# Performance work log

Measured on AMD Instinct MI355X. Metric: run time of the kernel, lower is better.

The kernel has to match this reference:

```python
import jax, jax.numpy as jnp
import numpy as np
import math

ALPHA = 0.5
DT = 0.1
DX = 1.0 / 128
KAPPA = 0.01

LAPL_OPS = [[[[0.34520446044393, 0.309591078922457, 0.34520446044393],
              [0.309591078922457, -2.619182157203629, 0.309591078922457],
              [0.34520446044393, 0.309591078922457, 0.34520446044393]]]]

T, C, H, W = 512, 2, 257, 257


def setup_inputs() -> dict:
    key = jax.random.key(0)
    k1, k2 = jax.random.split(key)
    output = jax.random.normal(k1, (T, C, H, W), dtype=jnp.float32)
    f1 = jax.random.normal(k2, (T, 1, H, W), dtype=jnp.float32)
    lap_kernel = jnp.asarray(LAPL_OPS, dtype=jnp.float32)  # (1,1,3,3), OIHW
    return {"output": output, "f1": f1, "lap_kernel": lap_kernel}


def _l1_weight_matrix(T_):
    # L1 fractional-derivative weights: w[j] = (j+1)^(1-a) - j^(1-a), j = 0..T-2
    a = ALPHA
    j = jnp.arange(T_ - 1, dtype=jnp.float32)
    w = (j + 1.0) ** (1.0 - a) - j ** (1.0 - a)  # w[0] = 1
    # dvec[m] = w[m-1] - w[m] for m >= 1 (m = i - k)
    dvec = jnp.concatenate([jnp.zeros((1,), jnp.float32), w[:-1] - w[1:]])
    i = jnp.arange(T_)[:, None]
    k = jnp.arange(T_)[None, :]
    diff = jnp.clip(i - k, 0, T_ - 2)
    M = jnp.where((i >= 1) & (k == i), 1.0, 0.0)                               # w0 * u_i
    M = M + jnp.where((k >= 1) & (k < i), -dvec[diff], 0.0)                    # -(w[i-k-1]-w[i-k]) u_k
    M = M + jnp.where((k == 0) & (i >= 1), -w[jnp.clip(i - 1, 0, T_ - 2)], 0.0)  # -w[i-1] u_0
    return M  # row 0 is all zeros, matching b[0] = 0


def reference(output, f1, lap_kernel):
    T_, _, H_, W_ = output.shape
    u = output[:, 0:1, :, :]                      # (T,1,H,W)
    u_flat = u.reshape(T_, H_ * W_)               # (T, N)

    # fractional time derivative as a single triangular matmul over time
    M = _l1_weight_matrix(T_)
    scale = DT ** (-ALPHA) / math.gamma(2.0 - ALPHA)
    D = (scale * (M @ u_flat)).reshape(T_, 1, H_, W_)

    # 3x3 Laplacian, VALID conv, divided by dx^2
    lap_u = jax.lax.conv_general_dilated(
        u, lap_kernel, window_strides=(1, 1), padding='VALID',
        dimension_numbers=('NCHW', 'OIHW', 'NCHW')) / (DX ** 2)

    res = (D[:, :, 1:-1, 1:-1] - KAPPA * lap_u
           + u[:, :, 1:-1, 1:-1] - f1[:, :, 1:-1, 1:-1])
    return jnp.mean(res ** 2)
```

## Files before the change

### kernel.cpp

```cpp
#include <hip/hip_runtime.h>

#define TT    512
#define WW    257
#define HWSZ  (WW*WW)
#define IMG2  (2*HWSZ)
#define SCALE 3.5682482323055424f
#define KD    163.84f

typedef short bf16x8 __attribute__((ext_vector_type(8)));
typedef short bf16x4 __attribute__((ext_vector_type(4)));
typedef float f32x4  __attribute__((ext_vector_type(4)));
typedef unsigned int u32x4 __attribute__((ext_vector_type(4)));

__device__ __forceinline__ float wf(int j) {
    return sqrtf((float)(j + 1)) - sqrtf((float)j);
}
__device__ __forceinline__ float mcoef(int i, int k) {
    if (i == 0 || k > i) return 0.f;
    if (k == i) return 1.f;
    if (k == 0) return -wf(i - 1);
    int d = i - k;
    return wf(d) - wf(d - 1);
}
__device__ __forceinline__ unsigned short f2b(float f) {
    unsigned u = __float_as_uint(f);
    return (unsigned short)((u + 0x7FFFu + ((u >> 16) & 1u)) >> 16);
}
__device__ __forceinline__ float b2f(unsigned short h) {
    return __uint_as_float(((unsigned)h) << 16);
}

__global__ __launch_bounds__(256)
void build_m(unsigned short* __restrict__ M, float* __restrict__ d_out) {
    int i = blockIdx.x;
    if (i == 0 && threadIdx.x == 0) *d_out = 0.f;
    for (int k = threadIdx.x; k < TT; k += 256)
        M[i * TT + k] = f2b(mcoef(i, k));
}

__global__ __launch_bounds__(512, 2)
void fused(const float* __restrict__ uin, const float* __restrict__ f1p,
           const float* __restrict__ lapk, const unsigned short* __restrict__ Mb,
           float* __restrict__ d_out)
{
    __shared__ unsigned short uS[2][128][64];
    __shared__ unsigned short sS[2][64][136];
    __shared__ float red[8];

    const int tid  = threadIdx.x;
    const int w    = tid >> 6;
    const int lane = tid & 63;
    const int lr   = lane & 15;
    const int lg   = lane >> 4;

    const int bid = blockIdx.x;
    const int wg  = (bid & 7) * 64 + (bid >> 3);
    const int xt  = wg >> 7;
    const int ypb = wg & 127;
    const int Y0  = 1 + 2 * ypb;
    const int c0  = xt * 64;
    const bool validB = (Y0 + 1) <= 255;

    const float ka = lapk[0], kb = lapk[1], kc = lapk[4];

    f32x4 acc0[8][2], acc1[8][2];
    #pragma unroll
    for (int a = 0; a < 8; ++a) {
        acc0[a][0] = (f32x4)0.f; acc0[a][1] = (f32x4)0.f;
        acc1[a][0] = (f32x4)0.f; acc1[a][1] = (f32x4)0.f;
    }

    const bool pad = (c0 + lane) == 255;
    const int  i00 = 32 * w;
    const int  i01 = 480 - 32 * w;
    const int  ec0 = w >> 1;
    const int  ec1 = (15 - w) >> 1;
    float lsum = 0.f;

    float a0[8], a1[8], a2[8], a3[8], fA[8], fB[8], ee;
    const int tl = lane >> 3, code = lane & 7, side = code >> 2, rj = code & 3;
    const size_t geoff = (size_t)tl * IMG2 + (size_t)(Y0 - 1 + rj) * WW
                       + (side ? c0 + 65 : c0);

    auto LOADR = [&](int c) {
        const int tb = 64 * c + 8 * w;
        const float* pu = uin + (size_t)tb * IMG2 + (size_t)(Y0 - 1) * WW + (c0 + 1) + lane;
        const float* pf = f1p + (size_t)tb * HWSZ + (size_t)Y0 * WW + (c0 + 1) + lane;
        #pragma unroll
        for (int rr = 0; rr < 8; ++rr) {
            const float* qu = pu + (size_t)rr * IMG2;
            a0[rr] = qu[0]; a1[rr] = qu[WW]; a2[rr] = qu[2 * WW]; a3[rr] = qu[3 * WW];
            fA[rr] = pf[(size_t)rr * HWSZ];
            fB[rr] = pf[(size_t)rr * HWSZ + WW];
        }
        ee = uin[(size_t)tb * IMG2 + geoff];
    };

    auto STAGE = [&](int b) {
        float e1  = __shfl(ee, lane + 1, 64);
        float e2  = __shfl(ee, lane + 2, 64);
        float QeX = fmaf(ka, ee + e2, kb * e1);
        u32x4 upA, upB;
        #pragma unroll
        for (int rr = 0; rr < 8; ++rr) {
            float PA = a0[rr] + a2[rr];
            float QA = fmaf(ka, PA, kb * a1[rr]);
            float RA = fmaf(kb, PA, kc * a1[rr]);
            float PB = a1[rr] + a3[rr];
            float QB = fmaf(ka, PB, kb * a2[rr]);
            float RB = fmaf(kb, PB, kc * a2[rr]);
            float qmA = __shfl(QA, lane - 1, 64), qpA = __shfl(QA, lane + 1, 64);
            float qmB = __shfl(QB, lane - 1, 64), qpB = __shfl(QB, lane + 1, 64);
            float eA0 = __shfl(QeX, 8 * rr,     64), eA1 = __shfl(QeX, 8 * rr + 4, 64);
            float eB0 = __shfl(QeX, 8 * rr + 1, 64), eB1 = __shfl(QeX, 8 * rr + 5, 64);
            if (lane == 0)  { qmA = eA0; qmB = eB0; }
            if (lane == 63) { qpA = eA1; qpB = eB1; }
            float lapA = qmA + qpA + RA;
            float lapB = qmB + qpB + RB;
            float sA = a1[rr] - fmaf(KD, lapA, fA[rr]);
            float sB_ = a2[rr] - fmaf(KD, lapB, fB[rr]);
            unsigned short uAv = pad ? (unsigned short)0 : f2b(a1[rr]);
            unsigned short sAv = pad ? (unsigned short)0 : f2b(sA);
            unsigned short uBv = (pad || !validB) ? (unsigned short)0 : f2b(a2[rr]);
            unsigned short sBv = (pad || !validB) ? (unsigned short)0 : f2b(sB_);
            sS[b][8 * w + rr][lane]      = sAv;
            sS[b][8 * w + rr][64 + lane] = sBv;
            if (rr & 1) { upA[rr >> 1] |= ((unsigned)uAv) << 16; upB[rr >> 1] |= ((unsigned)uBv) << 16; }
            else        { upA[rr >> 1]  = (unsigned)uAv;         upB[rr >> 1]  = (unsigned)uBv; }
        }
        *(u32x4*)&uS[b][lane]     [(w ^ (lane & 7)) * 8] = upA;
        *(u32x4*)&uS[b][64 + lane][(w ^ (lane & 7)) * 8] = upB;
    };

    auto EPI = [&](f32x4 (&acc)[8][2], int b, int lbase) {
        #pragma unroll
        for (int mi = 0; mi < 8; ++mi)
            #pragma unroll
            for (int nj = 0; nj < 2; ++nj) {
                bf16x4 sv = *(const bf16x4*)&sS[b][lbase + 16 * nj + lr][16 * mi + 4 * lg];
                #pragma unroll
                for (int r = 0; r < 4; ++r) {
                    float res = SCALE * acc[mi][nj][r] + b2f((unsigned short)sv[r]);
                    lsum += res * res;
                }
            }
    };

    LOADR(0);
    for (int c = 0; c < 8; ++c) {
        const int b = c & 1;

        bf16x8 m0a[2], m0b[2], m1a[2], m1b[2];
        #pragma unroll
        for (int sub = 0; sub < 2; ++sub) {
            const int s_ = 2 * c + sub;
            if (s_ <= w) {
                const unsigned short* mp0 = Mb + (size_t)(i00 + lr) * TT + 32 * s_ + 8 * lg;
                m0a[sub] = *(const bf16x8*)mp0; m0b[sub] = *(const bf16x8*)(mp0 + 16 * TT);
            }
            if (s_ <= 15 - w) {
                const unsigned short* mp1 = Mb + (size_t)(i01 + lr) * TT + 32 * s_ + 8 * lg;
                m1a[sub] = *(const bf16x8*)mp1; m1b[sub] = *(const bf16x8*)(mp1 + 16 * TT);
            }
        }
        __builtin_amdgcn_sched_barrier(0);

        STAGE(b);
        if (c < 7) LOADR(c + 1);

        __builtin_amdgcn_sched_barrier(0);
        asm volatile("s_waitcnt lgkmcnt(0)");
        __builtin_amdgcn_sched_barrier(0);
        __builtin_amdgcn_s_barrier();
        __builtin_amdgcn_sched_barrier(0);

        __builtin_amdgcn_s_setprio(1);
        #pragma unroll
        for (int sub = 0; sub < 2; ++sub) {
            const int s_ = 2 * c + sub;
            if (s_ <= w) {
                #pragma unroll
                for (int mi = 0; mi < 8; ++mi) {
                    bf16x8 a = *(const bf16x8*)&uS[b][16 * mi + lr][(((4 * sub + lg) ^ (lr & 7))) * 8];
                    acc0[mi][0] = __builtin_amdgcn_mfma_f32_16x16x32_bf16(a, m0a[sub], acc0[mi][0], 0, 0, 0);
                    acc0[mi][1] = __builtin_amdgcn_mfma_f32_16x16x32_bf16(a, m0b[sub], acc0[mi][1], 0, 0, 0);
                }
            }
            if (s_ <= 15 - w) {
                #pragma unroll
                for (int mi = 0; mi < 8; ++mi) {
                    bf16x8 a = *(const bf16x8*)&uS[b][16 * mi + lr][(((4 * sub + lg) ^ (lr & 7))) * 8];
                    acc1[mi][0] = __builtin_amdgcn_mfma_f32_16x16x32_bf16(a, m1a[sub], acc1[mi][0], 0, 0, 0);
                    acc1[mi][1] = __builtin_amdgcn_mfma_f32_16x16x32_bf16(a, m1b[sub], acc1[mi][1], 0, 0, 0);
                }
            }
        }
        __builtin_amdgcn_s_setprio(0);

        if (c == ec0) EPI(acc0, b, 32 * (w & 1));
        if (c == ec1) EPI(acc1, b, 32 * ((w + 1) & 1));
    }

    #pragma unroll
    for (int off = 32; off > 0; off >>= 1)
        lsum += __shfl_down(lsum, off, 64);
    if (lane == 0) red[w] = lsum;
    __syncthreads();
    if (tid == 0) {
        float tot = 0.f;
        #pragma unroll
        for (int q = 0; q < 8; ++q) tot += red[q];
        atomicAdd(d_out, tot * (1.0f / 33292800.0f));
    }
}

extern "C" void kernel_launch(void* const* d_in, const int* in_sizes, int n_in,
                              void* d_out, int out_size, void* d_ws, size_t ws_size,
                              hipStream_t stream)
{
    const float* uin  = (const float*)d_in[0];
    const float* f1   = (const float*)d_in[1];
    const float* lapk = (const float*)d_in[2];
    float* out = (float*)d_out;

    unsigned short* Mb = (unsigned short*)d_ws;

    build_m<<<dim3(TT), 256, 0, stream>>>(Mb, out);
    fused<<<dim3(512), 512, 0, stream>>>(uin, f1, lapk, Mb, out);
}
```

Before: 95.27 us.

## Software-pipeline staging so next tile is staged after MFMAs, loads two ahead

```diff
diff --git a/kernel.cpp b/kernel.cpp
--- a/kernel.cpp
+++ b/kernel.cpp
@@ -82,6 +82,8 @@
     const size_t geoff = (size_t)tl * IMG2 + (size_t)(Y0 - 1 + rj) * WW
                        + (side ? c0 + 65 : c0);
 
+    bf16x8 m0a[2], m0b[2], m1a[2], m1b[2];
+
     auto LOADR = [&](int c) {
         const int tb = 64 * c + 8 * w;
         const float* pu = uin + (size_t)tb * IMG2 + (size_t)(Y0 - 1) * WW + (c0 + 1) + lane;
@@ -94,6 +96,21 @@
             fB[rr] = pf[(size_t)rr * HWSZ + WW];
         }
         ee = uin[(size_t)tb * IMG2 + geoff];
+    };
+
+    auto MLOAD = [&](int k) {
+        #pragma unroll
+        for (int sub = 0; sub < 2; ++sub) {
+            const int s_ = 2 * k + sub;
+            if (s_ <= w) {
+                const unsigned short* mp0 = Mb + (size_t)(i00 + lr) * TT + 32 * s_ + 8 * lg;
+                m0a[sub] = *(const bf16x8*)mp0; m0b[sub] = *(const bf16x8*)(mp0 + 16 * TT);
+            }
+            if (s_ <= 15 - w) {
+                const unsigned short* mp1 = Mb + (size_t)(i01 + lr) * TT + 32 * s_ + 8 * lg;
+                m1a[sub] = *(const bf16x8*)mp1; m1b[sub] = *(const bf16x8*)(mp1 + 16 * TT);
+            }
+        }
     };
 
     auto STAGE = [&](int b) {
@@ -117,7 +134,7 @@
             if (lane == 63) { qpA = eA1; qpB = eB1; }
             float lapA = qmA + qpA + RA;
             float lapB = qmB + qpB + RB;
-            float sA = a1[rr] - fmaf(KD, lapA, fA[rr]);
+            float sA  = a1[rr] - fmaf(KD, lapA, fA[rr]);
             float sB_ = a2[rr] - fmaf(KD, lapB, fB[rr]);
             unsigned short uAv = pad ? (unsigned short)0 : f2b(a1[rr]);
             unsigned short sAv = pad ? (unsigned short)0 : f2b(sA);
@@ -147,37 +164,21 @@
     };
 
     LOADR(0);
-    for (int c = 0; c < 8; ++c) {
-        const int b = c & 1;
-
-        bf16x8 m0a[2], m0b[2], m1a[2], m1b[2];
+    MLOAD(0);
+    STAGE(0);
+    LOADR(1);
+    __builtin_amdgcn_sched_barrier(0);
+    asm volatile("s_waitcnt lgkmcnt(0)");
+    __builtin_amdgcn_sched_barrier(0);
+    __builtin_amdgcn_s_barrier();
+    __builtin_amdgcn_sched_barrier(0);
+
+    for (int k = 0; k < 8; ++k) {
+        const int b = k & 1;
+
         #pragma unroll
         for (int sub = 0; sub < 2; ++sub) {
-            const int s_ = 2 * c + sub;
-            if (s_ <= w) {
-                const unsigned short* mp0 = Mb + (size_t)(i00 + lr) * TT + 32 * s_ + 8 * lg;
-                m0a[sub] = *(const bf16x8*)mp0; m0b[sub] = *(const bf16x8*)(mp0 + 16 * TT);
-            }
-            if (s_ <= 15 - w) {
-                const unsigned short* mp1 = Mb + (size_t)(i01 + lr) * TT + 32 * s_ + 8 * lg;
-                m1a[sub] = *(const bf16x8*)mp1; m1b[sub] = *(const bf16x8*)(mp1 + 16 * TT);
-            }
-        }
-        __builtin_amdgcn_sched_barrier(0);
-
-        STAGE(b);
-        if (c < 7) LOADR(c + 1);
-
-        __builtin_amdgcn_sched_barrier(0);
-        asm volatile("s_waitcnt lgkmcnt(0)");
-        __builtin_amdgcn_sched_barrier(0);
-        __builtin_amdgcn_s_barrier();
-        __builtin_amdgcn_sched_barrier(0);
-
-        __builtin_amdgcn_s_setprio(1);
-        #pragma unroll
-        for (int sub = 0; sub < 2; ++sub) {
-            const int s_ = 2 * c + sub;
+            const int s_ = 2 * k + sub;
             if (s_ <= w) {
                 #pragma unroll
                 for (int mi = 0; mi < 8; ++mi) {
@@ -195,10 +196,20 @@
                 }
             }
         }
-        __builtin_amdgcn_s_setprio(0);
-
-        if (c == ec0) EPI(acc0, b, 32 * (w & 1));
-        if (c == ec1) EPI(acc1, b, 32 * ((w + 1) & 1));
+        if (k == ec0) EPI(acc0, b, 32 * (w & 1));
+        if (k == ec1) EPI(acc1, b, 32 * ((w + 1) & 1));
+
+        if (k < 7) {
+            STAGE(b ^ 1);
+            MLOAD(k + 1);
+            if (k < 6) LOADR(k + 2);
+
+            __builtin_amdgcn_sched_barrier(0);
+            asm volatile("s_waitcnt lgkmcnt(0)");
+            __builtin_amdgcn_sched_barrier(0);
+            __builtin_amdgcn_s_barrier();
+            __builtin_amdgcn_sched_barrier(0);
+        }
     }
 
     #pragma unroll
```

Result: slower. 97.78 us (+2.6%).

## Stage u tiles via async global_load_lds with finer-grained time-chunk pipeline

Applied to the files above, without the earlier changes.

```diff
diff --git a/kernel.cpp b/kernel.cpp
--- a/kernel.cpp
+++ b/kernel.cpp
@@ -10,7 +10,6 @@
 typedef short bf16x8 __attribute__((ext_vector_type(8)));
 typedef short bf16x4 __attribute__((ext_vector_type(4)));
 typedef float f32x4  __attribute__((ext_vector_type(4)));
-typedef unsigned int u32x4 __attribute__((ext_vector_type(4)));
 
 __device__ __forceinline__ float wf(int j) {
     return sqrtf((float)(j + 1)) - sqrtf((float)j);
@@ -29,6 +28,10 @@
 __device__ __forceinline__ float b2f(unsigned short h) {
     return __uint_as_float(((unsigned)h) << 16);
 }
+__device__ __forceinline__ void gl16(const float* g, float* l) {
+    __builtin_amdgcn_global_load_lds((const __attribute__((address_space(1))) void*)g,
+                                     (__attribute__((address_space(3))) void*)l, 16, 0, 0);
+}
 
 __global__ __launch_bounds__(256)
 void build_m(unsigned short* __restrict__ M, float* __restrict__ d_out) {
@@ -43,15 +46,13 @@
            const float* __restrict__ lapk, const unsigned short* __restrict__ Mb,
            float* __restrict__ d_out)
 {
-    __shared__ unsigned short uS[2][128][64];
-    __shared__ unsigned short sS[2][64][136];
+    __shared__ float          uRaw[2][16][272];
+    __shared__ unsigned short uS[2][128][32];
+    __shared__ unsigned short sS[2][32][136];
     __shared__ float red[8];
 
-    const int tid  = threadIdx.x;
-    const int w    = tid >> 6;
-    const int lane = tid & 63;
-    const int lr   = lane & 15;
-    const int lg   = lane >> 4;
+    const int tid = threadIdx.x, w = tid >> 6, lane = tid & 63;
+    const int lr = lane & 15, lg = lane >> 4;
 
     const int bid = blockIdx.x;
     const int wg  = (bid & 7) * 64 + (bid >> 3);
@@ -60,8 +61,11 @@
     const int Y0  = 1 + 2 * ypb;
     const int c0  = xt * 64;
     const bool validB = (Y0 + 1) <= 255;
+    const bool pad    = (c0 + lane) == 255;
 
     const float ka = lapk[0], kb = lapk[1], kc = lapk[4];
+    const int KA = (Y0 + c0) & 3;
+    const int i00 = 32 * w, i01 = 480 - 32 * w;
 
     f32x4 acc0[8][2], acc1[8][2];
     #pragma unroll
@@ -70,74 +74,114 @@
         acc1[a][0] = (f32x4)0.f; acc1[a][1] = (f32x4)0.f;
     }
 
-    const bool pad = (c0 + lane) == 255;
-    const int  i00 = 32 * w;
-    const int  i01 = 480 - 32 * w;
-    const int  ec0 = w >> 1;
-    const int  ec1 = (15 - w) >> 1;
+    const int rowmap  = lane / 17;
+    const int quadmap = lane - rowmap * 17;
+    const int etj = lane >> 3, eside = (lane >> 2) & 1, erj = lane & 3;
+
+    float fvv[2][4];
+    float eev[2];
+    bf16x8 m0a, m0b, m1a, m1b;
     float lsum = 0.f;
 
-    float a0[8], a1[8], a2[8], a3[8], fA[8], fB[8], ee;
-    const int tl = lane >> 3, code = lane & 7, side = code >> 2, rj = code & 3;
-    const size_t geoff = (size_t)tl * IMG2 + (size_t)(Y0 - 1 + rj) * WW
-                       + (side ? c0 + 65 : c0);
-
-    auto LOADR = [&](int c) {
-        const int tb = 64 * c + 8 * w;
-        const float* pu = uin + (size_t)tb * IMG2 + (size_t)(Y0 - 1) * WW + (c0 + 1) + lane;
-        const float* pf = f1p + (size_t)tb * HWSZ + (size_t)Y0 * WW + (c0 + 1) + lane;
-        #pragma unroll
-        for (int rr = 0; rr < 8; ++rr) {
-            const float* qu = pu + (size_t)rr * IMG2;
-            a0[rr] = qu[0]; a1[rr] = qu[WW]; a2[rr] = qu[2 * WW]; a3[rr] = qu[3 * WW];
-            fA[rr] = pf[(size_t)rr * HWSZ];
-            fB[rr] = pf[(size_t)rr * HWSZ + WW];
-        }
-        ee = uin[(size_t)tb * IMG2 + geoff];
-    };
-
-    auto STAGE = [&](int b) {
-        float e1  = __shfl(ee, lane + 1, 64);
-        float e2  = __shfl(ee, lane + 2, 64);
-        float QeX = fmaf(ka, ee + e2, kb * e1);
-        u32x4 upA, upB;
-        #pragma unroll
-        for (int rr = 0; rr < 8; ++rr) {
-            float PA = a0[rr] + a2[rr];
-            float QA = fmaf(ka, PA, kb * a1[rr]);
-            float RA = fmaf(kb, PA, kc * a1[rr]);
-            float PB = a1[rr] + a3[rr];
-            float QB = fmaf(ka, PB, kb * a2[rr]);
-            float RB = fmaf(kb, PB, kc * a2[rr]);
+    auto ISSUE_STAGE = [&](int k, int b) {
+        #pragma unroll
+        for (int j = 0; j < 2; ++j) {
+            const int t  = 16 * k + 2 * w + j;
+            const int tl = 2 * w + j;
+            size_t bl = (size_t)t * IMG2 + (size_t)(Y0 - 1 + rowmap) * WW + (c0 + 1);
+            gl16(uin + (bl & ~(size_t)3) + 4 * quadmap, &uRaw[b][tl][0]);
+            size_t b3 = (size_t)t * IMG2 + (size_t)(Y0 + 2) * WW + (c0 + 1);
+            if (lane < 4)
+                gl16(uin + (b3 & ~(size_t)3) + 4 * (13 + lane), &uRaw[b][tl][256]);
+            size_t fb = (size_t)t * HWSZ + (size_t)Y0 * WW + (c0 + 1) + lane;
+            fvv[b][2 * j]     = f1p[fb];
+            fvv[b][2 * j + 1] = f1p[fb + WW];
+        }
+    };
+    auto ISSUE_EE = [&](int K0, int eb) {
+        const int t = 16 * (K0 + (etj >> 1)) + 2 * w + (etj & 1);
+        eev[eb] = uin[(size_t)t * IMG2 + (size_t)(Y0 - 1 + erj) * WW + (eside ? c0 + 65 : c0)];
+    };
+    auto MLOAD = [&](int s) {
+        const int s0 = (s <= w) ? s : w;
+        const int s1 = (s <= 15 - w) ? s : 15 - w;
+        const unsigned short* mp0 = Mb + (size_t)(i00 + lr) * TT + 32 * s0 + 8 * lg;
+        const unsigned short* mp1 = Mb + (size_t)(i01 + lr) * TT + 32 * s1 + 8 * lg;
+        m0a = *(const bf16x8*)mp0; m0b = *(const bf16x8*)(mp0 + 16 * TT);
+        m1a = *(const bf16x8*)mp1; m1b = *(const bf16x8*)(mp1 + 16 * TT);
+    };
+
+    auto STAGE = [&](int k, int b, int p, int e, int eb, int i4) {
+        const float ee = eev[eb];
+        float e1 = __shfl(ee, lane + 1, 64);
+        float e2 = __shfl(ee, lane + 2, 64);
+        float Qe = fmaf(ka, ee + e2, kb * e1);
+        unsigned packA = 0, packB = 0;
+        #pragma unroll
+        for (int j = 0; j < 2; ++j) {
+            const int t  = 16 * k + 2 * w + j;
+            const int tl = 2 * w + j;
+            const int aa0 = (2 * t + KA) & 3;
+            const int aa1 = (aa0 + 1) & 3, aa2 = (aa0 + 2) & 3, aa3 = (aa0 + 3) & 3;
+            float a0 = uRaw[b][tl][      lane + aa0];
+            float a1 = uRaw[b][tl][ 68 + lane + aa1];
+            float a2 = uRaw[b][tl][136 + lane + aa2];
+            float a3 = uRaw[b][tl][204 + lane + aa3];
+            float fA = fvv[b][2 * j], fB = fvv[b][2 * j + 1];
+            float PA = a0 + a2, QA = fmaf(ka, PA, kb * a1), RA = fmaf(kb, PA, kc * a1);
+            float PB = a1 + a3, QB = fmaf(ka, PB, kb * a2), RB = fmaf(kb, PB, kc * a2);
             float qmA = __shfl(QA, lane - 1, 64), qpA = __shfl(QA, lane + 1, 64);
             float qmB = __shfl(QB, lane - 1, 64), qpB = __shfl(QB, lane + 1, 64);
-            float eA0 = __shfl(QeX, 8 * rr,     64), eA1 = __shfl(QeX, 8 * rr + 4, 64);
-            float eB0 = __shfl(QeX, 8 * rr + 1, 64), eB1 = __shfl(QeX, 8 * rr + 5, 64);
+            const int tj = 2 * i4 + j;
+            float eA0 = __shfl(Qe, 8 * tj, 64),     eA1 = __shfl(Qe, 8 * tj + 4, 64);
+            float eB0 = __shfl(Qe, 8 * tj + 1, 64), eB1 = __shfl(Qe, 8 * tj + 5, 64);
             if (lane == 0)  { qmA = eA0; qmB = eB0; }
             if (lane == 63) { qpA = eA1; qpB = eB1; }
-            float lapA = qmA + qpA + RA;
-            float lapB = qmB + qpB + RB;
-            float sA = a1[rr] - fmaf(KD, lapA, fA[rr]);
-            float sB_ = a2[rr] - fmaf(KD, lapB, fB[rr]);
-            unsigned short uAv = pad ? (unsigned short)0 : f2b(a1[rr]);
+            float lapA = qmA + qpA + RA, lapB = qmB + qpB + RB;
+            float sA  = a1 - fmaf(KD, lapA, fA);
+            float sB_ = a2 - fmaf(KD, lapB, fB);
+            unsigned short uAv = pad ? (unsigned short)0 : f2b(a1);
             unsigned short sAv = pad ? (unsigned short)0 : f2b(sA);
-            unsigned short uBv = (pad || !validB) ? (unsigned short)0 : f2b(a2[rr]);
+            unsigned short uBv = (pad || !validB) ? (unsigned short)0 : f2b(a2);
             unsigned short sBv = (pad || !validB) ? (unsigned short)0 : f2b(sB_);
-            sS[b][8 * w + rr][lane]      = sAv;
-            sS[b][8 * w + rr][64 + lane] = sBv;
-            if (rr & 1) { upA[rr >> 1] |= ((unsigned)uAv) << 16; upB[rr >> 1] |= ((unsigned)uBv) << 16; }
-            else        { upA[rr >> 1]  = (unsigned)uAv;         upB[rr >> 1]  = (unsigned)uBv; }
-        }
-        *(u32x4*)&uS[b][lane]     [(w ^ (lane & 7)) * 8] = upA;
-        *(u32x4*)&uS[b][64 + lane][(w ^ (lane & 7)) * 8] = upB;
-    };
-
-    auto EPI = [&](f32x4 (&acc)[8][2], int b, int lbase) {
+            sS[p][16 * e + tl][lane]      = sAv;
+            sS[p][16 * e + tl][64 + lane] = sBv;
+            if (j == 0) { packA = uAv; packB = uBv; }
+            else        { packA |= ((unsigned)uAv) << 16; packB |= ((unsigned)uBv) << 16; }
+        }
+        const unsigned off = (unsigned)((32 * e + 4 * w) ^ ((lane & 3) << 4));
+        *(unsigned*)((char*)&uS[p][lane][0]      + off) = packA;
+        *(unsigned*)((char*)&uS[p][64 + lane][0] + off) = packB;
+    };
+
+    auto MMA = [&](int s, int p) {
+        bf16x8 af[8];
+        #pragma unroll
+        for (int mi = 0; mi < 8; ++mi)
+            af[mi] = *(const bf16x8*)((char*)&uS[p][16 * mi + lr][0]
+                                      + ((16 * lg) ^ ((lr & 3) << 4)));
+        if (s <= w) {
+            #pragma unroll
+            for (int mi = 0; mi < 8; ++mi) {
+                acc0[mi][0] = __builtin_amdgcn_mfma_f32_16x16x32_bf16(af[mi], m0a, acc0[mi][0], 0, 0, 0);
+                acc0[mi][1] = __builtin_amdgcn_mfma_f32_16x16x32_bf16(af[mi], m0b, acc0[mi][1], 0, 0, 0);
+            }
+        }
+        if (s <= 15 - w) {
+            #pragma unroll
+            for (int mi = 0; mi < 8; ++mi) {
+                acc1[mi][0] = __builtin_amdgcn_mfma_f32_16x16x32_bf16(af[mi], m1a, acc1[mi][0], 0, 0, 0);
+                acc1[mi][1] = __builtin_amdgcn_mfma_f32_16x16x32_bf16(af[mi], m1b, acc1[mi][1], 0, 0, 0);
+            }
+        }
+    };
+
+    auto EPI = [&](f32x4 (&acc)[8][2], int pp) {
         #pragma unroll
         for (int mi = 0; mi < 8; ++mi)
             #pragma unroll
             for (int nj = 0; nj < 2; ++nj) {
-                bf16x4 sv = *(const bf16x4*)&sS[b][lbase + 16 * nj + lr][16 * mi + 4 * lg];
+                bf16x4 sv = *(const bf16x4*)&sS[pp][16 * nj + lr][16 * mi + 4 * lg];
                 #pragma unroll
                 for (int r = 0; r < 4; ++r) {
                     float res = SCALE * acc[mi][nj][r] + b2f((unsigned short)sv[r]);
@@ -146,59 +190,46 @@
             }
     };
 
-    LOADR(0);
-    for (int c = 0; c < 8; ++c) {
-        const int b = c & 1;
-
-        bf16x8 m0a[2], m0b[2], m1a[2], m1b[2];
-        #pragma unroll
-        for (int sub = 0; sub < 2; ++sub) {
-            const int s_ = 2 * c + sub;
-            if (s_ <= w) {
-                const unsigned short* mp0 = Mb + (size_t)(i00 + lr) * TT + 32 * s_ + 8 * lg;
-                m0a[sub] = *(const bf16x8*)mp0; m0b[sub] = *(const bf16x8*)(mp0 + 16 * TT);
-            }
-            if (s_ <= 15 - w) {
-                const unsigned short* mp1 = Mb + (size_t)(i01 + lr) * TT + 32 * s_ + 8 * lg;
-                m1a[sub] = *(const bf16x8*)mp1; m1b[sub] = *(const bf16x8*)(mp1 + 16 * TT);
-            }
-        }
-        __builtin_amdgcn_sched_barrier(0);
-
-        STAGE(b);
-        if (c < 7) LOADR(c + 1);
-
-        __builtin_amdgcn_sched_barrier(0);
-        asm volatile("s_waitcnt lgkmcnt(0)");
-        __builtin_amdgcn_sched_barrier(0);
-        __builtin_amdgcn_s_barrier();
-        __builtin_amdgcn_sched_barrier(0);
-
-        __builtin_amdgcn_s_setprio(1);
-        #pragma unroll
-        for (int sub = 0; sub < 2; ++sub) {
-            const int s_ = 2 * c + sub;
-            if (s_ <= w) {
-                #pragma unroll
-                for (int mi = 0; mi < 8; ++mi) {
-                    bf16x8 a = *(const bf16x8*)&uS[b][16 * mi + lr][(((4 * sub + lg) ^ (lr & 7))) * 8];
-                    acc0[mi][0] = __builtin_amdgcn_mfma_f32_16x16x32_bf16(a, m0a[sub], acc0[mi][0], 0, 0, 0);
-                    acc0[mi][1] = __builtin_amdgcn_mfma_f32_16x16x32_bf16(a, m0b[sub], acc0[mi][1], 0, 0, 0);
-                }
-            }
-            if (s_ <= 15 - w) {
-                #pragma unroll
-                for (int mi = 0; mi < 8; ++mi) {
-                    bf16x8 a = *(const bf16x8*)&uS[b][16 * mi + lr][(((4 * sub + lg) ^ (lr & 7))) * 8];
-                    acc1[mi][0] = __builtin_amdgcn_mfma_f32_16x16x32_bf16(a, m1a[sub], acc1[mi][0], 0, 0, 0);
-                    acc1[mi][1] = __builtin_amdgcn_mfma_f32_16x16x32_bf16(a, m1b[sub], acc1[mi][1], 0, 0, 0);
-                }
-            }
-        }
-        __builtin_amdgcn_s_setprio(0);
-
-        if (c == ec0) EPI(acc0, b, 32 * (w & 1));
-        if (c == ec1) EPI(acc1, b, 32 * ((w + 1) & 1));
+    ISSUE_EE(0, 0);
+    ISSUE_STAGE(0, 0);
+
+    for (int kb = 0; kb < 4; ++kb) {
+        #pragma unroll
+        for (int jj = 0; jj < 8; ++jj) {
+            const int k  = 8 * kb + jj;
+            const int b  = jj & 1;
+            const int p  = (jj >> 1) & 1;
+            const int e  = jj & 1;
+            const int eb = (jj >> 2) & 1;
+            const int i4 = jj & 3;
+
+            if ((jj & 1) == 0) MLOAD(k >> 1);
+            if (k < 31) {
+                if ((jj & 3) == 3) ISSUE_EE(k + 1, (jj == 3) ? 1 : 0);
+                ISSUE_STAGE(k + 1, b ^ 1);
+            }
+            __builtin_amdgcn_sched_barrier(0);
+            if (k == 31)             asm volatile("s_waitcnt vmcnt(0)");
+            else if ((jj & 3) == 0)  asm volatile("s_waitcnt vmcnt(12)");
+            else if ((jj & 3) == 1)  asm volatile("s_waitcnt vmcnt(8)");
+            else if ((jj & 3) == 2)  asm volatile("s_waitcnt vmcnt(12)");
+            else                     asm volatile("s_waitcnt vmcnt(9)");
+            __builtin_amdgcn_sched_barrier(0);
+
+            STAGE(k, b, p, e, eb, i4);
+
+            __builtin_amdgcn_sched_barrier(0);
+            asm volatile("s_waitcnt lgkmcnt(0)");
+            __builtin_amdgcn_sched_barrier(0);
+            __builtin_amdgcn_s_barrier();
+            __builtin_amdgcn_sched_barrier(0);
+
+            if (jj & 1) {
+                MMA(k >> 1, p);
+                if (k == 2 * w + 1)  EPI(acc0, w & 1);
+                if (k == 31 - 2 * w) EPI(acc1, (15 - w) & 1);
+            }
+        }
     }
 
     #pragma unroll
```

After: 133.7 us. 1.4x slower.

## Pack row pairs into bf16x2 words to halve shuffles and LDS stores

Applied to the files above, without the earlier changes.

```diff
diff --git a/kernel.cpp b/kernel.cpp
--- a/kernel.cpp
+++ b/kernel.cpp
@@ -8,7 +8,6 @@
 #define KD    163.84f
 
 typedef short bf16x8 __attribute__((ext_vector_type(8)));
-typedef short bf16x4 __attribute__((ext_vector_type(4)));
 typedef float f32x4  __attribute__((ext_vector_type(4)));
 typedef unsigned int u32x4 __attribute__((ext_vector_type(4)));
 
@@ -26,9 +25,11 @@
     unsigned u = __float_as_uint(f);
     return (unsigned short)((u + 0x7FFFu + ((u >> 16) & 1u)) >> 16);
 }
-__device__ __forceinline__ float b2f(unsigned short h) {
-    return __uint_as_float(((unsigned)h) << 16);
-}
+__device__ __forceinline__ unsigned pk2(float A, float B) {
+    return (unsigned)f2b(A) | ((unsigned)f2b(B) << 16);
+}
+__device__ __forceinline__ float lo2f(unsigned u) { return __uint_as_float(u << 16); }
+__device__ __forceinline__ float hi2f(unsigned u) { return __uint_as_float(u & 0xFFFF0000u); }
 
 __global__ __launch_bounds__(256)
 void build_m(unsigned short* __restrict__ M, float* __restrict__ d_out) {
@@ -44,7 +45,8 @@
            float* __restrict__ d_out)
 {
     __shared__ unsigned short uS[2][128][64];
-    __shared__ unsigned short sS[2][64][136];
+    __shared__ unsigned       sS32[2][64][66];
+    __shared__ unsigned       eQ[2][8][16];
     __shared__ float red[8];
 
     const int tid  = threadIdx.x;
@@ -60,6 +62,7 @@
     const int Y0  = 1 + 2 * ypb;
     const int c0  = xt * 64;
     const bool validB = (Y0 + 1) <= 255;
+    const bool pad    = (c0 + lane) == 255;
 
     const float ka = lapk[0], kb = lapk[1], kc = lapk[4];
 
@@ -70,7 +73,6 @@
         acc1[a][0] = (f32x4)0.f; acc1[a][1] = (f32x4)0.f;
     }
 
-    const bool pad = (c0 + lane) == 255;
     const int  i00 = 32 * w;
     const int  i01 = 480 - 32 * w;
     const int  ec0 = w >> 1;
@@ -78,9 +80,11 @@
     float lsum = 0.f;
 
     float a0[8], a1[8], a2[8], a3[8], fA[8], fB[8], ee;
-    const int tl = lane >> 3, code = lane & 7, side = code >> 2, rj = code & 3;
-    const size_t geoff = (size_t)tl * IMG2 + (size_t)(Y0 - 1 + rj) * WW
-                       + (side ? c0 + 65 : c0);
+    const int etl = lane >> 3, eside = (lane >> 2) & 1, erow = lane & 3;
+    const size_t geoff = (size_t)etl * IMG2 + (size_t)(Y0 - 1 + erow) * WW
+                       + (eside ? c0 + 65 : c0);
+
+    bf16x8 m0a[2], m0b[2], m1a[2], m1b[2];
 
     auto LOADR = [&](int c) {
         const int tb = 64 * c + 8 * w;
@@ -97,9 +101,17 @@
     };
 
     auto STAGE = [&](int b) {
-        float e1  = __shfl(ee, lane + 1, 64);
-        float e2  = __shfl(ee, lane + 2, 64);
-        float QeX = fmaf(ka, ee + e2, kb * e1);
+        unsigned* eQw = &eQ[b][w][0];
+        {
+            const int sb8 = ((lane & 15) >> 1) * 8 + (lane & 1) * 4;
+            float v0 = __shfl(ee, sb8, 64);
+            float v1 = __shfl(ee, sb8 + 1, 64);
+            float v2 = __shfl(ee, sb8 + 2, 64);
+            float v3 = __shfl(ee, sb8 + 3, 64);
+            float QeA = fmaf(ka, v0 + v2, kb * v1);
+            float QeB = fmaf(ka, v1 + v3, kb * v2);
+            if (lane < 16) eQw[lane] = pk2(QeA, QeB);
+        }
         u32x4 upA, upB;
         #pragma unroll
         for (int rr = 0; rr < 8; ++rr) {
@@ -109,27 +121,27 @@
             float PB = a1[rr] + a3[rr];
             float QB = fmaf(ka, PB, kb * a2[rr]);
             float RB = fmaf(kb, PB, kc * a2[rr]);
-            float qmA = __shfl(QA, lane - 1, 64), qpA = __shfl(QA, lane + 1, 64);
-            float qmB = __shfl(QB, lane - 1, 64), qpB = __shfl(QB, lane + 1, 64);
-            float eA0 = __shfl(QeX, 8 * rr,     64), eA1 = __shfl(QeX, 8 * rr + 4, 64);
-            float eB0 = __shfl(QeX, 8 * rr + 1, 64), eB1 = __shfl(QeX, 8 * rr + 5, 64);
-            if (lane == 0)  { qmA = eA0; qmB = eB0; }
-            if (lane == 63) { qpA = eA1; qpB = eB1; }
-            float lapA = qmA + qpA + RA;
-            float lapB = qmB + qpB + RB;
-            float sA = a1[rr] - fmaf(KD, lapA, fA[rr]);
+            unsigned Qp = pk2(QA, QB);
+            unsigned pm = __shfl((int)Qp, lane - 1, 64);
+            unsigned pp = __shfl((int)Qp, lane + 1, 64);
+            unsigned ep = eQw[2 * rr + (lane == 63 ? 1 : 0)];
+            if (lane == 0)  pm = ep;
+            if (lane == 63) pp = ep;
+            float lapA = lo2f(pm) + lo2f(pp) + RA;
+            float lapB = hi2f(pm) + hi2f(pp) + RB;
+            float sA  = a1[rr] - fmaf(KD, lapA, fA[rr]);
             float sB_ = a2[rr] - fmaf(KD, lapB, fB[rr]);
+            unsigned short sAv = pad ? (unsigned short)0 : f2b(sA);
+            unsigned short sBv = (pad || !validB) ? (unsigned short)0 : f2b(sB_);
+            sS32[b][8 * w + rr][lane] = (unsigned)sAv | ((unsigned)sBv << 16);
             unsigned short uAv = pad ? (unsigned short)0 : f2b(a1[rr]);
-            unsigned short sAv = pad ? (unsigned short)0 : f2b(sA);
             unsigned short uBv = (pad || !validB) ? (unsigned short)0 : f2b(a2[rr]);
-            unsigned short sBv = (pad || !validB) ? (unsigned short)0 : f2b(sB_);
-            sS[b][8 * w + rr][lane]      = sAv;
-            sS[b][8 * w + rr][64 + lane] = sBv;
             if (rr & 1) { upA[rr >> 1] |= ((unsigned)uAv) << 16; upB[rr >> 1] |= ((unsigned)uBv) << 16; }
             else        { upA[rr >> 1]  = (unsigned)uAv;         upB[rr >> 1]  = (unsigned)uBv; }
         }
-        *(u32x4*)&uS[b][lane]     [(w ^ (lane & 7)) * 8] = upA;
-        *(u32x4*)&uS[b][64 + lane][(w ^ (lane & 7)) * 8] = upB;
+        const int swz = (w ^ (lane & 7)) * 8;
+        *(u32x4*)&uS[b][2 * lane][swz]     = upA;
+        *(u32x4*)&uS[b][2 * lane + 1][swz] = upB;
     };
 
     auto EPI = [&](f32x4 (&acc)[8][2], int b, int lbase) {
@@ -137,12 +149,14 @@
         for (int mi = 0; mi < 8; ++mi)
             #pragma unroll
             for (int nj = 0; nj < 2; ++nj) {
-                bf16x4 sv = *(const bf16x4*)&sS[b][lbase + 16 * nj + lr][16 * mi + 4 * lg];
-                #pragma unroll
-                for (int r = 0; r < 4; ++r) {
-                    float res = SCALE * acc[mi][nj][r] + b2f((unsigned short)sv[r]);
-                    lsum += res * res;
-                }
+                const unsigned* sp = &sS32[b][lbase + 16 * nj + lr][8 * mi + 2 * lg];
+                unsigned s0 = sp[0], s1 = sp[1];
+                f32x4 a = acc[mi][nj];
+                float r0 = fmaf(SCALE, a[0], lo2f(s0));
+                float r1 = fmaf(SCALE, a[1], hi2f(s0));
+                float r2 = fmaf(SCALE, a[2], lo2f(s1));
+                float r3 = fmaf(SCALE, a[3], hi2f(s1));
+                lsum += r0 * r0 + r1 * r1 + r2 * r2 + r3 * r3;
             }
     };
 
@@ -150,7 +164,6 @@
     for (int c = 0; c < 8; ++c) {
         const int b = c & 1;
 
-        bf16x8 m0a[2], m0b[2], m1a[2], m1b[2];
         #pragma unroll
         for (int sub = 0; sub < 2; ++sub) {
             const int s_ = 2 * c + sub;
```

New measurement: 96.27 us. About the same (+1.0%).
